# Optimization experiments

Measured on AMD Instinct MI355X. Metric: run time of the kernel, lower is better.

## Reference

```python
import jax, jax.numpy as jnp
import numpy as np

N = 50000        # nodes
E = 1_600_000    # edges (avg degree 32)
IN_DIM = 128
NUM_CONFS = 16
CONF_EMB = 4
HIDDEN = 64
OUT = 32


def setup_inputs() -> dict:
    key = jax.random.key(0)
    ks = jax.random.split(key, 8)
    x = jax.random.normal(ks[0], (N, IN_DIM), jnp.float32)
    conf_ids = jax.random.randint(ks[1], (N,), 0, NUM_CONFS)
    edge_index = jax.random.randint(ks[2], (2, E), 0, N)
    edge_weight = jax.random.uniform(ks[3], (E,), jnp.float32)
    # learned params
    conf_table = jax.random.normal(ks[4], (NUM_CONFS, CONF_EMB), jnp.float32) * 0.1
    W1 = jax.random.normal(ks[5], (IN_DIM + CONF_EMB, HIDDEN), jnp.float32) / np.sqrt(IN_DIM + CONF_EMB)
    b1 = jnp.zeros((HIDDEN,), jnp.float32)
    W2 = jax.random.normal(ks[6], (HIDDEN, OUT), jnp.float32) / np.sqrt(HIDDEN)
    b2 = jnp.zeros((OUT,), jnp.float32)
    return dict(x=x, conf_ids=conf_ids, edge_index=edge_index, edge_weight=edge_weight,
                conf_table=conf_table, W1=W1, b1=b1, W2=W2, b2=b2)


def _gcn_conv(h, W, b, row, col, w, n):
    """PyG GCNConv: symmetric norm with self-loops (loops already appended to row/col/w)."""
    deg = jax.ops.segment_sum(w, col, num_segments=n)              # weighted in-degree [N]
    dinv = jnp.where(deg > 0, jax.lax.rsqrt(deg), 0.0)             # D^{-1/2}
    norm = dinv[row] * w * dinv[col]                               # per-edge coefficient [E+N]
    hW = h @ W                                                     # [N, out]
    out = jax.ops.segment_sum(hW[row] * norm[:, None], col, num_segments=n)
    return out + b


def reference(x, conf_ids, edge_index, edge_weight, conf_table, W1, b1, W2, b2):
    row, col = edge_index[0], edge_index[1]
    # add self-loops once (same math for both conv layers)
    loop = jnp.arange(N)
    row = jnp.concatenate([row, loop])
    col = jnp.concatenate([col, loop])
    w = jnp.concatenate([edge_weight, jnp.ones((N,), edge_weight.dtype)])

    h = jnp.concatenate([x, conf_table[conf_ids]], axis=-1)        # [N, in+conf_emb]
    h = jax.nn.relu(_gcn_conv(h, W1, b1, row, col, w, N))
    return _gcn_conv(h, W2, b2, row, col, w, N)
```

## Files before the change

### kernel.cpp

```cpp
#include <hip/hip_runtime.h>
#include <hip/hip_fp16.h>

#define BKT_SHIFT 8
#define BKT_SIZE  256
#define SEGCAP    12544
#define EPB       4096
#define EPT       16
#define NT        64

__global__ void k_zero(int* __restrict__ cursor) {
    cursor[threadIdx.x] = 0;
}

__global__ void k_binA(const int* __restrict__ row, const int* __restrict__ col,
                       const float* __restrict__ w, int* __restrict__ cursor,
                       uint2* __restrict__ seg, int e) {
    __shared__ int hist[256];
    __shared__ int base[256];
    __shared__ int rank[256];
    int t = threadIdx.x;
    hist[t] = 0; rank[t] = 0;
    __syncthreads();
    int b0 = blockIdx.x * EPB;
    unsigned pay[EPT]; unsigned cc[EPT];
#pragma unroll
    for (int k = 0; k < EPT; ++k) {
        int i = b0 + k * 256 + t;
        if (i < e) {
            unsigned r  = (unsigned)row[i];
            unsigned c  = (unsigned)col[i];
            unsigned wq = (unsigned)__half_as_ushort(__float2half_rn(w[i]));
            pay[k] = r | (wq << 16);
            cc[k] = c;
            atomicAdd(&hist[c >> BKT_SHIFT], 1);
        } else cc[k] = 0xFFFFFFFFu;
    }
    __syncthreads();
    if (hist[t] > 0) base[t] = atomicAdd(&cursor[t], hist[t]);
    __syncthreads();
#pragma unroll
    for (int k = 0; k < EPT; ++k) {
        if (cc[k] != 0xFFFFFFFFu) {
            int b = cc[k] >> BKT_SHIFT;
            int pos = base[b] + atomicAdd(&rank[b], 1);
            if (pos < SEGCAP)
                seg[(size_t)b * SEGCAP + pos] = make_uint2(pay[k], cc[k] & (BKT_SIZE - 1));
        }
    }
}

__global__ void k_binB(const int* __restrict__ cursor, const uint2* __restrict__ seg,
                       unsigned* __restrict__ csr, int* __restrict__ begs,
                       int* __restrict__ cnts, float* __restrict__ dinv, int n) {
    __shared__ int hist[BKT_SIZE];
    __shared__ float wsumf[BKT_SIZE];
    __shared__ int begL[BKT_SIZE];
    __shared__ int rank[BKT_SIZE];
    __shared__ unsigned pay[SEGCAP];
    int b = blockIdx.x;
    int t = threadIdx.x;
    int nodes = min(BKT_SIZE, n - b * BKT_SIZE);
    int count = min(cursor[b], SEGCAP);
    hist[t] = 0; wsumf[t] = 0.f; rank[t] = 0;
    __syncthreads();
    const uint2* sp = seg + (size_t)b * SEGCAP;
    for (int i = t; i < count; i += 256) {
        uint2 r = sp[i];
        atomicAdd(&hist[r.y], 1);
        atomicAdd(&wsumf[r.y], __half2float(__ushort_as_half((unsigned short)(r.x >> 16))));
    }
    __syncthreads();
    int v = hist[t];
    int vpad = (v + 15) & ~15;
    begL[t] = vpad;
    __syncthreads();
    for (int off = 1; off < 256; off <<= 1) {
        int tv = (t >= off) ? begL[t - off] : 0;
        __syncthreads();
        begL[t] += tv;
        __syncthreads();
    }
    int beg_excl = begL[t] - vpad;
    int ptot = min(begL[255], SEGCAP);
    __syncthreads();
    begL[t] = beg_excl;
    __syncthreads();
    if (t < nodes) {
        int node = b * BKT_SIZE + t;
        begs[node] = b * SEGCAP + beg_excl;
        cnts[node] = vpad;
        dinv[node] = rsqrtf(1.0f + wsumf[t]);
    }
    for (int i = t; i < ptot; i += 256) pay[i] = 0u;
    __syncthreads();
    for (int i = t; i < count; i += 256) {
        uint2 r = sp[i];
        int pos = begL[r.y] + atomicAdd(&rank[r.y], 1);
        if (pos < SEGCAP) pay[pos] = r.x;
    }
    __syncthreads();
    unsigned* cp = csr + (size_t)b * SEGCAP;
    for (int i = t; i < ptot; i += 256) cp[i] = pay[i];
}

__global__ void k_hw1(const float* __restrict__ x, const int* __restrict__ conf_ids,
                      const float* __restrict__ conf_table, const float* __restrict__ W1,
                      const float* __restrict__ dinv, __half* __restrict__ hW1s, int n) {
    __shared__ float xs[NT][128];
    __shared__ float cemb[NT][4];
    int t = threadIdx.x;
    int base = blockIdx.x * NT;
    for (int q = t; q < NT * 32; q += 256) {
        int node = base + (q >> 5);
        int k4 = (q & 31) * 4;
        float4 v = make_float4(0.f, 0.f, 0.f, 0.f);
        if (node < n) v = *(const float4*)(x + (size_t)node * 128 + k4);
        *(float4*)&xs[q >> 5][k4] = v;
    }
    if (t < NT) {
        int node = base + t;
        int cid = (node < n) ? conf_ids[node] : 0;
        float4 ce = *(const float4*)(conf_table + cid * 4);
        if (node >= n) ce = make_float4(0.f, 0.f, 0.f, 0.f);
        *(float4*)&cemb[t][0] = ce;
    }
    __syncthreads();
    int w = t >> 6, f = t & 63;
    int nb = w * 16;
    float acc[16];
#pragma unroll
    for (int m = 0; m < 16; ++m) acc[m] = 0.f;
    for (int kq = 0; kq < 32; ++kq) {
        int k = kq * 4;
        float w1a = W1[(k + 0) * 64 + f];
        float w1b = W1[(k + 1) * 64 + f];
        float w1c = W1[(k + 2) * 64 + f];
        float w1d = W1[(k + 3) * 64 + f];
#pragma unroll
        for (int m = 0; m < 16; ++m) {
            float4 xv = *(const float4*)&xs[nb + m][k];
            acc[m] += xv.x * w1a + xv.y * w1b + xv.z * w1c + xv.w * w1d;
        }
    }
    float wca = W1[128 * 64 + f], wcb = W1[129 * 64 + f];
    float wcc = W1[130 * 64 + f], wcd = W1[131 * 64 + f];
#pragma unroll
    for (int m = 0; m < 16; ++m) {
        float4 ce = *(const float4*)&cemb[nb + m][0];
        acc[m] += ce.x * wca + ce.y * wcb + ce.z * wcc + ce.w * wcd;
    }
#pragma unroll
    for (int m = 0; m < 16; ++m) {
        int node = base + nb + m;
        if (node < n) hW1s[(size_t)node * 64 + f] = __float2half_rn(acc[m] * dinv[node]);
    }
}

__global__ void k_agg1(const __half* __restrict__ hW1s, const int* __restrict__ begs,
                       const int* __restrict__ cnts, const unsigned* __restrict__ csr,
                       const float* __restrict__ dinv, const float* __restrict__ b1,
                       const float* __restrict__ W2, __half* __restrict__ hW2s, int n) {
    __shared__ float h1s[8][64];
    int t = threadIdx.x;
    int q  = t >> 5;
    int hl = t & 31;
    int nid = blockIdx.x * 8 + q;
    const half2* __restrict__ hrow = (const half2*)hW1s;
    float dn = 0.f;
    float2 sf = make_float2(0.f, 0.f);
    int c = 0;
    const unsigned* sp = csr;
    if (nid < n) {
        dn = dinv[nid];
        c = cnts[nid];
        sp = csr + begs[nid];
        sf = __half22float2(hrow[(size_t)nid * 32 + hl]);
    }
    float a0 = 0.f, a1 = 0.f;
    const half2 hz = __float2half2_rn(0.f);
    uint4 s0 = *(const uint4*)(sp);
    uint4 s1 = *(const uint4*)(sp + 4);
    uint4 s2 = *(const uint4*)(sp + 8);
    uint4 s3 = *(const uint4*)(sp + 12);
    for (int j = 0; j < c; j += 16) {
        uint4 n0 = *(const uint4*)(sp + j + 16);
        uint4 n1 = *(const uint4*)(sp + j + 20);
        uint4 n2 = *(const uint4*)(sp + j + 24);
        uint4 n3 = *(const uint4*)(sp + j + 28);
        half2 acc0 = hz, acc1 = hz, acc2 = hz, acc3 = hz;
#define STEP1(s, A) { half2 vv = hrow[(size_t)((s) & 0xffffu) * 32 + hl]; \
                      half2 ww = __half2half2(__ushort_as_half((unsigned short)((s) >> 16))); \
                      A = __hfma2(vv, ww, A); }
        STEP1(s0.x, acc0) STEP1(s0.y, acc1) STEP1(s0.z, acc2) STEP1(s0.w, acc3)
        STEP1(s1.x, acc0) STEP1(s1.y, acc1) STEP1(s1.z, acc2) STEP1(s1.w, acc3)
        STEP1(s2.x, acc0) STEP1(s2.y, acc1) STEP1(s2.z, acc2) STEP1(s2.w, acc3)
        STEP1(s3.x, acc0) STEP1(s3.y, acc1) STEP1(s3.z, acc2) STEP1(s3.w, acc3)
#undef STEP1
        float2 f0 = __half22float2(acc0);
        float2 f1 = __half22float2(acc1);
        float2 f2 = __half22float2(acc2);
        float2 f3 = __half22float2(acc3);
        a0 += (f0.x + f1.x) + (f2.x + f3.x);
        a1 += (f0.y + f1.y) + (f2.y + f3.y);
        s0 = n0; s1 = n1; s2 = n2; s3 = n3;
    }
    float2 bb = *(const float2*)(b1 + 2 * hl);
    float h0  = fmaxf((sf.x + a0) * dn + bb.x, 0.0f);
    float h1v = fmaxf((sf.y + a1) * dn + bb.y, 0.0f);
    if (nid >= n) { h0 = 0.f; h1v = 0.f; }
    *(float2*)&h1s[q][2 * hl] = make_float2(h0, h1v);
    __syncthreads();
    float s = 0.f;
#pragma unroll
    for (int k = 0; k < 64; k += 4) {
        float4 hv = *(const float4*)&h1s[q][k];
        s += hv.x * W2[(k + 0) * 32 + hl];
        s += hv.y * W2[(k + 1) * 32 + hl];
        s += hv.z * W2[(k + 2) * 32 + hl];
        s += hv.w * W2[(k + 3) * 32 + hl];
    }
    if (nid < n) hW2s[(size_t)nid * 32 + hl] = __float2half_rn(s * dn);
}

__global__ void k_agg2(const __half* __restrict__ hW2s, const int* __restrict__ begs,
                       const int* __restrict__ cnts, const unsigned* __restrict__ csr,
                       const float* __restrict__ dinv, const float* __restrict__ b2,
                       float* __restrict__ out, int n) {
    int t = threadIdx.x;
    int g  = t >> 4;
    int hl = t & 15;
    int nid = blockIdx.x * 16 + g;
    const half2* __restrict__ hrow = (const half2*)hW2s;
    float dn = 0.f;
    float2 sf = make_float2(0.f, 0.f);
    int c = 0;
    const unsigned* sp = csr;
    if (nid < n) {
        dn = dinv[nid];
        c = cnts[nid];
        sp = csr + begs[nid];
        sf = __half22float2(hrow[(size_t)nid * 16 + hl]);
    }
    float a0 = 0.f, a1 = 0.f;
    const half2 hz = __float2half2_rn(0.f);
    uint4 s0 = *(const uint4*)(sp);
    uint4 s1 = *(const uint4*)(sp + 4);
    uint4 s2 = *(const uint4*)(sp + 8);
    uint4 s3 = *(const uint4*)(sp + 12);
    for (int j = 0; j < c; j += 16) {
        uint4 n0 = *(const uint4*)(sp + j + 16);
        uint4 n1 = *(const uint4*)(sp + j + 20);
        uint4 n2 = *(const uint4*)(sp + j + 24);
        uint4 n3 = *(const uint4*)(sp + j + 28);
        half2 acc0 = hz, acc1 = hz, acc2 = hz, acc3 = hz;
#define STEP2(s, A) { half2 vv = hrow[(size_t)((s) & 0xffffu) * 16 + hl]; \
                      half2 ww = __half2half2(__ushort_as_half((unsigned short)((s) >> 16))); \
                      A = __hfma2(vv, ww, A); }
        STEP2(s0.x, acc0) STEP2(s0.y, acc1) STEP2(s0.z, acc2) STEP2(s0.w, acc3)
        STEP2(s1.x, acc0) STEP2(s1.y, acc1) STEP2(s1.z, acc2) STEP2(s1.w, acc3)
        STEP2(s2.x, acc0) STEP2(s2.y, acc1) STEP2(s2.z, acc2) STEP2(s2.w, acc3)
        STEP2(s3.x, acc0) STEP2(s3.y, acc1) STEP2(s3.z, acc2) STEP2(s3.w, acc3)
#undef STEP2
        float2 f0 = __half22float2(acc0);
        float2 f1 = __half22float2(acc1);
        float2 f2 = __half22float2(acc2);
        float2 f3 = __half22float2(acc3);
        a0 += (f0.x + f1.x) + (f2.x + f3.x);
        a1 += (f0.y + f1.y) + (f2.y + f3.y);
        s0 = n0; s1 = n1; s2 = n2; s3 = n3;
    }
    if (nid < n) {
        float2 bb = *(const float2*)(b2 + 2 * hl);
        float o0 = (sf.x + a0) * dn + bb.x;
        float o1 = (sf.y + a1) * dn + bb.y;
        *(float2*)&out[(size_t)nid * 32 + 2 * hl] = make_float2(o0, o1);
    }
}

extern "C" void kernel_launch(void* const* d_in, const int* in_sizes, int n_in,
                              void* d_out, int out_size, void* d_ws, size_t ws_size,
                              hipStream_t stream) {
    const float* x          = (const float*)d_in[0];
    const int*   conf_ids   = (const int*)  d_in[1];
    const int*   eidx       = (const int*)  d_in[2];
    const float* ew         = (const float*)d_in[3];
    const float* conf_table = (const float*)d_in[4];
    const float* W1         = (const float*)d_in[5];
    const float* b1         = (const float*)d_in[6];
    const float* W2         = (const float*)d_in[7];
    const float* b2         = (const float*)d_in[8];
    float* out = (float*)d_out;

    const int n = in_sizes[1];
    const int e = in_sizes[3];
    const int* row = eidx;
    const int* col = eidx + e;
    const int nbkt = (n + BKT_SIZE - 1) / BKT_SIZE;

    char* ws = (char*)d_ws;
    size_t off = 0;
    auto alloc = [&](size_t bytes) -> char* {
        char* p = ws + off;
        off = (off + bytes + 255) & ~(size_t)255;
        return p;
    };
    int*      cursor = (int*)     alloc(256 * 4);
    uint2*    seg    = (uint2*)   alloc((size_t)nbkt * SEGCAP * 8);
    unsigned* csr    = (unsigned*)alloc((size_t)nbkt * SEGCAP * 4);
    int*      begs   = (int*)     alloc((size_t)n * 4);
    int*      cnts   = (int*)     alloc((size_t)n * 4);
    float*    dinv   = (float*)   alloc((size_t)n * 4);
    __half*   hW2s   = (__half*)  alloc((size_t)n * 32 * 2);
    __half*   hW1s   = (__half*)seg;

    const int B = 256;
    int ga  = (e + EPB - 1) / EPB;
    int gt  = (n + NT - 1) / NT;
    int g8  = (n + 7) / 8;
    int g16 = (n + 15) / 16;

    k_zero<<<1,    B, 0, stream>>>(cursor);
    k_binA<<<ga,   B, 0, stream>>>(row, col, ew, cursor, seg, e);
    k_binB<<<nbkt, B, 0, stream>>>(cursor, seg, csr, begs, cnts, dinv, n);
    k_hw1 <<<gt,   B, 0, stream>>>(x, conf_ids, conf_table, W1, dinv, hW1s, n);
    k_agg1<<<g8,   B, 0, stream>>>(hW1s, begs, cnts, csr, dinv, b1, W2, hW2s, n);
    k_agg2<<<g16,  B, 0, stream>>>(hW2s, begs, cnts, csr, dinv, b2, out, n);
}
```

Baseline: 135.9 us.

## Run X·W1 GEMM concurrently with edge binning and apply dinv in binB

The feature transform X·W1 no longer depends on dinv, so it moves into the same launch as the edge-binning pass, with block indices past ga doing the GEMM. The dinv row scaling moves into the tail of k_binB, which reads the unscaled half-precision hW1 back and rewrites it scaled. This removes one kernel launch and lets the compute-bound GEMM overlap with the atomic-heavy binning. In exchange, hW1 needs its own buffer instead of aliasing seg, and scaling adds an extra read-modify-write pass over hW1 plus a second fp16 rounding; the GEMM tile also shrinks from 64 to 32 nodes.

Result: faster. 131.5 us (-3.2%).

```diff
diff --git a/kernel.cpp b/kernel.cpp
--- a/kernel.cpp
+++ b/kernel.cpp
@@ -6,52 +6,107 @@
 #define SEGCAP    12544
 #define EPB       4096
 #define EPT       16
-#define NT        64
+#define NT2       32
 
 __global__ void k_zero(int* __restrict__ cursor) {
     cursor[threadIdx.x] = 0;
 }
 
-__global__ void k_binA(const int* __restrict__ row, const int* __restrict__ col,
-                       const float* __restrict__ w, int* __restrict__ cursor,
-                       uint2* __restrict__ seg, int e) {
-    __shared__ int hist[256];
-    __shared__ int base[256];
-    __shared__ int rank[256];
+struct ShA { int hist[256]; int base[256]; int rank[256]; };
+struct ShB { float xs[NT2][128]; float cemb[NT2][4]; };
+
+__global__ void k_binA_hw1(const int* __restrict__ row, const int* __restrict__ col,
+                           const float* __restrict__ w, int* __restrict__ cursor,
+                           uint2* __restrict__ seg,
+                           const float* __restrict__ x, const int* __restrict__ conf_ids,
+                           const float* __restrict__ conf_table, const float* __restrict__ W1,
+                           __half* __restrict__ hW1, int e, int n, int ga) {
+    __shared__ __align__(16) char shraw[sizeof(ShB)];
     int t = threadIdx.x;
-    hist[t] = 0; rank[t] = 0;
-    __syncthreads();
-    int b0 = blockIdx.x * EPB;
-    unsigned pay[EPT]; unsigned cc[EPT];
-#pragma unroll
-    for (int k = 0; k < EPT; ++k) {
-        int i = b0 + k * 256 + t;
-        if (i < e) {
-            unsigned r  = (unsigned)row[i];
-            unsigned c  = (unsigned)col[i];
-            unsigned wq = (unsigned)__half_as_ushort(__float2half_rn(w[i]));
-            pay[k] = r | (wq << 16);
-            cc[k] = c;
-            atomicAdd(&hist[c >> BKT_SHIFT], 1);
-        } else cc[k] = 0xFFFFFFFFu;
-    }
-    __syncthreads();
-    if (hist[t] > 0) base[t] = atomicAdd(&cursor[t], hist[t]);
-    __syncthreads();
-#pragma unroll
-    for (int k = 0; k < EPT; ++k) {
-        if (cc[k] != 0xFFFFFFFFu) {
-            int b = cc[k] >> BKT_SHIFT;
-            int pos = base[b] + atomicAdd(&rank[b], 1);
-            if (pos < SEGCAP)
-                seg[(size_t)b * SEGCAP + pos] = make_uint2(pay[k], cc[k] & (BKT_SIZE - 1));
+    if ((int)blockIdx.x < ga) {
+        ShA& A = *reinterpret_cast<ShA*>(shraw);
+        A.hist[t] = 0; A.rank[t] = 0;
+        __syncthreads();
+        int b0 = blockIdx.x * EPB;
+        unsigned pay[EPT]; unsigned cc[EPT];
+#pragma unroll
+        for (int k = 0; k < EPT; ++k) {
+            int i = b0 + k * 256 + t;
+            if (i < e) {
+                unsigned r  = (unsigned)row[i];
+                unsigned c  = (unsigned)col[i];
+                unsigned wq = (unsigned)__half_as_ushort(__float2half_rn(w[i]));
+                pay[k] = r | (wq << 16);
+                cc[k] = c;
+                atomicAdd(&A.hist[c >> BKT_SHIFT], 1);
+            } else cc[k] = 0xFFFFFFFFu;
+        }
+        __syncthreads();
+        if (A.hist[t] > 0) A.base[t] = atomicAdd(&cursor[t], A.hist[t]);
+        __syncthreads();
+#pragma unroll
+        for (int k = 0; k < EPT; ++k) {
+            if (cc[k] != 0xFFFFFFFFu) {
+                int b = cc[k] >> BKT_SHIFT;
+                int pos = A.base[b] + atomicAdd(&A.rank[b], 1);
+                if (pos < SEGCAP)
+                    seg[(size_t)b * SEGCAP + pos] = make_uint2(pay[k], cc[k] & (BKT_SIZE - 1));
+            }
+        }
+    } else {
+        ShB& B = *reinterpret_cast<ShB*>(shraw);
+        int base = (blockIdx.x - ga) * NT2;
+        for (int q = t; q < NT2 * 32; q += 256) {
+            int node = base + (q >> 5);
+            int k4 = (q & 31) * 4;
+            float4 v = make_float4(0.f, 0.f, 0.f, 0.f);
+            if (node < n) v = *(const float4*)(x + (size_t)node * 128 + k4);
+            *(float4*)&B.xs[q >> 5][k4] = v;
+        }
+        if (t < NT2) {
+            int node = base + t;
+            int cid = (node < n) ? conf_ids[node] : 0;
+            float4 ce = *(const float4*)(conf_table + cid * 4);
+            if (node >= n) ce = make_float4(0.f, 0.f, 0.f, 0.f);
+            *(float4*)&B.cemb[t][0] = ce;
+        }
+        __syncthreads();
+        int wv = t >> 6, f = t & 63;
+        int nb = wv * 8;
+        float acc[8];
+#pragma unroll
+        for (int m = 0; m < 8; ++m) acc[m] = 0.f;
+        for (int kq = 0; kq < 32; ++kq) {
+            int k = kq * 4;
+            float w1a = W1[(k + 0) * 64 + f];
+            float w1b = W1[(k + 1) * 64 + f];
+            float w1c = W1[(k + 2) * 64 + f];
+            float w1d = W1[(k + 3) * 64 + f];
+#pragma unroll
+            for (int m = 0; m < 8; ++m) {
+                float4 xv = *(const float4*)&B.xs[nb + m][k];
+                acc[m] += xv.x * w1a + xv.y * w1b + xv.z * w1c + xv.w * w1d;
+            }
+        }
+        float wca = W1[128 * 64 + f], wcb = W1[129 * 64 + f];
+        float wcc = W1[130 * 64 + f], wcd = W1[131 * 64 + f];
+#pragma unroll
+        for (int m = 0; m < 8; ++m) {
+            float4 ce = *(const float4*)&B.cemb[nb + m][0];
+            acc[m] += ce.x * wca + ce.y * wcb + ce.z * wcc + ce.w * wcd;
+        }
+#pragma unroll
+        for (int m = 0; m < 8; ++m) {
+            int node = base + nb + m;
+            if (node < n) hW1[(size_t)node * 64 + f] = __float2half_rn(acc[m]);
         }
     }
 }
 
 __global__ void k_binB(const int* __restrict__ cursor, const uint2* __restrict__ seg,
                        unsigned* __restrict__ csr, int* __restrict__ begs,
-                       int* __restrict__ cnts, float* __restrict__ dinv, int n) {
+                       int* __restrict__ cnts, float* __restrict__ dinv,
+                       __half* __restrict__ hW1, int n) {
     __shared__ int hist[BKT_SIZE];
     __shared__ float wsumf[BKT_SIZE];
     __shared__ int begL[BKT_SIZE];
@@ -84,12 +139,14 @@
     int ptot = min(begL[255], SEGCAP);
     __syncthreads();
     begL[t] = beg_excl;
-    __syncthreads();
+    float dv = rsqrtf(1.0f + wsumf[t]);
+    __syncthreads();
+    wsumf[t] = dv;
     if (t < nodes) {
         int node = b * BKT_SIZE + t;
         begs[node] = b * SEGCAP + beg_excl;
         cnts[node] = vpad;
-        dinv[node] = rsqrtf(1.0f + wsumf[t]);
+        dinv[node] = dv;
     }
     for (int i = t; i < ptot; i += 256) pay[i] = 0u;
     __syncthreads();
@@ -101,58 +158,12 @@
     __syncthreads();
     unsigned* cp = csr + (size_t)b * SEGCAP;
     for (int i = t; i < ptot; i += 256) cp[i] = pay[i];
-}
-
-__global__ void k_hw1(const float* __restrict__ x, const int* __restrict__ conf_ids,
-                      const float* __restrict__ conf_table, const float* __restrict__ W1,
-                      const float* __restrict__ dinv, __half* __restrict__ hW1s, int n) {
-    __shared__ float xs[NT][128];
-    __shared__ float cemb[NT][4];
-    int t = threadIdx.x;
-    int base = blockIdx.x * NT;
-    for (int q = t; q < NT * 32; q += 256) {
-        int node = base + (q >> 5);
-        int k4 = (q & 31) * 4;
-        float4 v = make_float4(0.f, 0.f, 0.f, 0.f);
-        if (node < n) v = *(const float4*)(x + (size_t)node * 128 + k4);
-        *(float4*)&xs[q >> 5][k4] = v;
-    }
-    if (t < NT) {
-        int node = base + t;
-        int cid = (node < n) ? conf_ids[node] : 0;
-        float4 ce = *(const float4*)(conf_table + cid * 4);
-        if (node >= n) ce = make_float4(0.f, 0.f, 0.f, 0.f);
-        *(float4*)&cemb[t][0] = ce;
-    }
-    __syncthreads();
-    int w = t >> 6, f = t & 63;
-    int nb = w * 16;
-    float acc[16];
-#pragma unroll
-    for (int m = 0; m < 16; ++m) acc[m] = 0.f;
-    for (int kq = 0; kq < 32; ++kq) {
-        int k = kq * 4;
-        float w1a = W1[(k + 0) * 64 + f];
-        float w1b = W1[(k + 1) * 64 + f];
-        float w1c = W1[(k + 2) * 64 + f];
-        float w1d = W1[(k + 3) * 64 + f];
-#pragma unroll
-        for (int m = 0; m < 16; ++m) {
-            float4 xv = *(const float4*)&xs[nb + m][k];
-            acc[m] += xv.x * w1a + xv.y * w1b + xv.z * w1c + xv.w * w1d;
-        }
-    }
-    float wca = W1[128 * 64 + f], wcb = W1[129 * 64 + f];
-    float wcc = W1[130 * 64 + f], wcd = W1[131 * 64 + f];
-#pragma unroll
-    for (int m = 0; m < 16; ++m) {
-        float4 ce = *(const float4*)&cemb[nb + m][0];
-        acc[m] += ce.x * wca + ce.y * wcb + ce.z * wcc + ce.w * wcd;
-    }
-#pragma unroll
-    for (int m = 0; m < 16; ++m) {
-        int node = base + nb + m;
-        if (node < n) hW1s[(size_t)node * 64 + f] = __float2half_rn(acc[m] * dinv[node]);
+    half2* hp = (half2*)(hW1 + (size_t)b * BKT_SIZE * 64);
+    int lim = nodes * 32;
+    for (int i = t; i < lim; i += 256) {
+        float dn = wsumf[i >> 5];
+        float2 f = __half22float2(hp[i]);
+        hp[i] = __floats2half2_rn(f.x * dn, f.y * dn);
     }
 }
 
@@ -311,18 +322,18 @@
     int*      cnts   = (int*)     alloc((size_t)n * 4);
     float*    dinv   = (float*)   alloc((size_t)n * 4);
     __half*   hW2s   = (__half*)  alloc((size_t)n * 32 * 2);
-    __half*   hW1s   = (__half*)seg;
+    __half*   hW1    = (__half*)  alloc((size_t)n * 64 * 2);
 
     const int B = 256;
     int ga  = (e + EPB - 1) / EPB;
-    int gt  = (n + NT - 1) / NT;
+    int gw  = (n + NT2 - 1) / NT2;
     int g8  = (n + 7) / 8;
     int g16 = (n + 15) / 16;
 
-    k_zero<<<1,    B, 0, stream>>>(cursor);
-    k_binA<<<ga,   B, 0, stream>>>(row, col, ew, cursor, seg, e);
-    k_binB<<<nbkt, B, 0, stream>>>(cursor, seg, csr, begs, cnts, dinv, n);
-    k_hw1 <<<gt,   B, 0, stream>>>(x, conf_ids, conf_table, W1, dinv, hW1s, n);
-    k_agg1<<<g8,   B, 0, stream>>>(hW1s, begs, cnts, csr, dinv, b1, W2, hW2s, n);
-    k_agg2<<<g16,  B, 0, stream>>>(hW2s, begs, cnts, csr, dinv, b2, out, n);
-}
+    k_zero    <<<1,        B, 0, stream>>>(cursor);
+    k_binA_hw1<<<ga + gw,  B, 0, stream>>>(row, col, ew, cursor, seg,
+                                           x, conf_ids, conf_table, W1, hW1, e, n, ga);
+    k_binB    <<<nbkt,     B, 0, stream>>>(cursor, seg, csr, begs, cnts, dinv, hW1, n);
+    k_agg1    <<<g8,       B, 0, stream>>>(hW1, begs, cnts, csr, dinv, b1, W2, hW2s, n);
+    k_agg2    <<<g16,      B, 0, stream>>>(hW2s, begs, cnts, csr, dinv, b2, out, n);
+}
```

## Stage edge binning in shared memory for coalesced bucket writes

Applied to the files above, without the earlier changes.

The binning kernel now does a block-local prefix scan over bucket histograms. It stages each block's edges in shared memory sorted by bucket, then writes them out in contiguous runs per bucket instead of scattering each edge directly to global memory. This targets uncoalesced global scatter writes during CSR construction. The cost is an extra scan pass and about 32KB of shared memory per block, which may lower occupancy. The first-layer hidden buffer also gets its own allocation instead of aliasing the segment buffer, and one redundant barrier is removed from the second binning kernel.

New measurement: 133.5 us. About the same (-1.7%).

```diff
diff --git a/kernel.cpp b/kernel.cpp
--- a/kernel.cpp
+++ b/kernel.cpp
@@ -16,13 +16,16 @@
                        const float* __restrict__ w, int* __restrict__ cursor,
                        uint2* __restrict__ seg, int e) {
     __shared__ int hist[256];
-    __shared__ int base[256];
+    __shared__ int begL[256];
+    __shared__ int gbase[256];
     __shared__ int rank[256];
+    __shared__ uint2 pay[EPB];
     int t = threadIdx.x;
     hist[t] = 0; rank[t] = 0;
     __syncthreads();
     int b0 = blockIdx.x * EPB;
-    unsigned pay[EPT]; unsigned cc[EPT];
+    int cnt_local = min(EPB, e - b0);
+    unsigned pv[EPT]; unsigned cc[EPT];
 #pragma unroll
     for (int k = 0; k < EPT; ++k) {
         int i = b0 + k * 256 + t;
@@ -30,22 +33,41 @@
             unsigned r  = (unsigned)row[i];
             unsigned c  = (unsigned)col[i];
             unsigned wq = (unsigned)__half_as_ushort(__float2half_rn(w[i]));
-            pay[k] = r | (wq << 16);
+            pv[k] = r | (wq << 16);
             cc[k] = c;
             atomicAdd(&hist[c >> BKT_SHIFT], 1);
         } else cc[k] = 0xFFFFFFFFu;
     }
     __syncthreads();
-    if (hist[t] > 0) base[t] = atomicAdd(&cursor[t], hist[t]);
+    int v = hist[t];
+    begL[t] = v;
+    __syncthreads();
+    for (int off = 1; off < 256; off <<= 1) {
+        int tv = (t >= off) ? begL[t - off] : 0;
+        __syncthreads();
+        begL[t] += tv;
+        __syncthreads();
+    }
+    int excl = begL[t] - v;
+    __syncthreads();
+    begL[t] = excl;
+    if (v > 0) gbase[t] = atomicAdd(&cursor[t], v);
     __syncthreads();
 #pragma unroll
     for (int k = 0; k < EPT; ++k) {
         if (cc[k] != 0xFFFFFFFFu) {
             int b = cc[k] >> BKT_SHIFT;
-            int pos = base[b] + atomicAdd(&rank[b], 1);
-            if (pos < SEGCAP)
-                seg[(size_t)b * SEGCAP + pos] = make_uint2(pay[k], cc[k] & (BKT_SIZE - 1));
+            int pos = begL[b] + atomicAdd(&rank[b], 1);
+            pay[pos] = make_uint2(pv[k], ((unsigned)b << 8) | (cc[k] & (BKT_SIZE - 1)));
         }
+    }
+    __syncthreads();
+    for (int i = t; i < cnt_local; i += 256) {
+        uint2 r = pay[i];
+        int b = r.y >> 8;
+        int gidx = gbase[b] + (i - begL[b]);
+        if (gidx < SEGCAP)
+            seg[(size_t)b * SEGCAP + gidx] = make_uint2(r.x, r.y & (BKT_SIZE - 1));
     }
 }
 
@@ -84,7 +106,6 @@
     int ptot = min(begL[255], SEGCAP);
     __syncthreads();
     begL[t] = beg_excl;
-    __syncthreads();
     if (t < nodes) {
         int node = b * BKT_SIZE + t;
         begs[node] = b * SEGCAP + beg_excl;
@@ -311,7 +332,7 @@
     int*      cnts   = (int*)     alloc((size_t)n * 4);
     float*    dinv   = (float*)   alloc((size_t)n * 4);
     __half*   hW2s   = (__half*)  alloc((size_t)n * 32 * 2);
-    __half*   hW1s   = (__half*)seg;
+    __half*   hW1s   = (__half*)  alloc((size_t)n * 64 * 2);
 
     const int B = 256;
     int ga  = (e + EPB - 1) / EPB;
```
